# Kernel optimization log

Measured on AMD Instinct MI355X. Metric: run time of the kernel, lower is better.

Reference implementation:

```python
import jax, jax.numpy as jnp
import numpy as np

GROUPS = 32
EPS = 1e-6


def group_norm(x, gamma, beta):
    b, h, w, c = x.shape
    xg = x.reshape(b, h, w, GROUPS, c // GROUPS)
    mean = jnp.mean(xg, axis=(1, 2, 4), keepdims=True)
    var = jnp.var(xg, axis=(1, 2, 4), keepdims=True)
    xg = (xg - mean) * jax.lax.rsqrt(var + EPS)
    return xg.reshape(b, h, w, c) * gamma + beta


def setup_inputs() -> dict:
    key = jax.random.key(0)
    ks = jax.random.split(key, 6)
    B, H, W, C = 4, 64, 64, 512
    scale = 0.02
    return {
        "x": jax.random.normal(ks[0], (B, H, W, C), dtype=jnp.float32),
        "gamma": jnp.ones((C,), dtype=jnp.float32),
        "beta": jnp.zeros((C,), dtype=jnp.float32),
        "wq": jax.random.normal(ks[1], (C, C), dtype=jnp.float32) * scale,
        "bq": jnp.zeros((C,), dtype=jnp.float32),
        "wk": jax.random.normal(ks[2], (C, C), dtype=jnp.float32) * scale,
        "bk": jnp.zeros((C,), dtype=jnp.float32),
        "wv": jax.random.normal(ks[3], (C, C), dtype=jnp.float32) * scale,
        "bv": jnp.zeros((C,), dtype=jnp.float32),
        "wo": jax.random.normal(ks[4], (C, C), dtype=jnp.float32) * scale,
        "bo": jnp.zeros((C,), dtype=jnp.float32),
    }


def reference(x, gamma, beta, wq, bq, wk, bk, wv, bv, wo, bo):
    b, h, w, c = x.shape
    xn = group_norm(x, gamma, beta)
    # 1x1 convs == per-pixel linear layers
    q = (jnp.einsum('bhwc,cd->bhwd', xn, wq) + bq).reshape(b, h * w, c)
    k = (jnp.einsum('bhwc,cd->bhwd', xn, wk) + bk).reshape(b, h * w, c)
    v = (jnp.einsum('bhwc,cd->bhwd', xn, wv) + bv).reshape(b, h * w, c)
    # full (hw x hw) attention, single head
    scores = jnp.einsum('bic,bjc->bij', q, k) * (c ** -0.5)  # [b, hw, hw]
    attn = jax.nn.softmax(scores, axis=-1)
    out = jnp.einsum('bij,bjc->bic', attn, v).reshape(b, h, w, c)
    return jnp.einsum('bhwc,cd->bhwd', out, wo) + bo + x
```

## Files before the change

kernel.cpp:

```cpp
#include <hip/hip_runtime.h>
#include <stdint.h>


typedef __attribute__((ext_vector_type(8))) short bf16x8;
typedef __attribute__((ext_vector_type(8))) unsigned short u16x8;
typedef __attribute__((ext_vector_type(4))) float f32x4;

#define SOFTMAX_SCALE 0.044194173824159216f

__device__ __forceinline__ unsigned short f2bf(float f) {
  unsigned int x = __float_as_uint(f);
  x += 0x7fffu + ((x >> 16) & 1u);
  return (unsigned short)(x >> 16);
}
__device__ __forceinline__ float bf2f(unsigned short u) {
  return __uint_as_float((unsigned int)u << 16);
}

__device__ __forceinline__ void gl_lds16(const void* g, void* l) {
  __builtin_amdgcn_global_load_lds(
      (__attribute__((address_space(1))) unsigned char*)g,
      (__attribute__((address_space(3))) unsigned char*)l, 16, 0, 0);
}

__device__ __forceinline__ void gemm_tile(
    const unsigned short* __restrict__ A, long lda,
    const unsigned short* __restrict__ B, long ldb,
    int K, unsigned short* As, unsigned short* Bs, f32x4 acc[4][4]) {
  const int tid = threadIdx.x;
  const int wave = tid >> 6, lane = tid & 63;
  const int srow = lane >> 3;
  const int soff = ((lane & 7) ^ srow) * 16;
  const int wm = (wave >> 1) * 64, wn = (wave & 1) * 64;
  const int lrow = lane & 15;
  const int rsw = lrow & 7;
  const int kgb = lane >> 4;

  for (int k0 = 0; k0 < K; k0 += 64) {
    __syncthreads();
    for (int i = 0; i < 4; ++i) {
      int chunk = wave * 4 + i;
      int row = chunk * 8 + srow;
      gl_lds16((const char*)(A + (long)row * lda + k0) + soff, (char*)As + chunk * 1024);
      gl_lds16((const char*)(B + (long)row * ldb + k0) + soff, (char*)Bs + chunk * 1024);
    }
    __syncthreads();
#pragma unroll
    for (int ks = 0; ks < 2; ++ks) {
      bf16x8 af[4], bfr[4];
      const int off = ((ks * 4 + kgb) ^ rsw) * 8;
#pragma unroll
      for (int t = 0; t < 4; ++t) {
        af[t]  = *(const bf16x8*)&As[(wm + t * 16 + lrow) * 64 + off];
        bfr[t] = *(const bf16x8*)&Bs[(wn + t * 16 + lrow) * 64 + off];
      }
#pragma unroll
      for (int mt = 0; mt < 4; ++mt)
#pragma unroll
        for (int nt = 0; nt < 4; ++nt)
          acc[mt][nt] = __builtin_amdgcn_mfma_f32_16x16x32_bf16(af[mt], bfr[nt], acc[mt][nt], 0, 0, 0);
    }
  }
}

#define EPILOG_SETUP                                          \
  const int lane = threadIdx.x & 63, wave = threadIdx.x >> 6; \
  const int wm = (wave >> 1) * 64, wn = (wave & 1) * 64;      \
  const int lcol = lane & 15, lrb = (lane >> 4) * 4;

__global__ void prep_kernel(const float* __restrict__ wq, const float* __restrict__ wk,
                            const float* __restrict__ wv, const float* __restrict__ wo,
                            const float* __restrict__ bq, const float* __restrict__ bk,
                            const float* __restrict__ bv,
                            unsigned short* __restrict__ wqkvT,
                            unsigned short* __restrict__ woT,
                            float* __restrict__ bias, float* __restrict__ stats,
                            float* __restrict__ lsum) {
  long id = (long)blockIdx.x * 256 + threadIdx.x;
  if (id < 786432) {
    long n = id >> 9, k = id & 511;
    const float* w = (n < 512) ? wq : (n < 1024 ? wk : wv);
    wqkvT[id] = f2bf(w[k * 512 + (n & 511)]);
  } else if (id < 786432 + 262144) {
    long j = id - 786432, n = j >> 9, k = j & 511;
    woT[j] = f2bf(wo[k * 512 + n]);
  } else if (id < 786432 + 262144 + 1536) {
    long j = id - 786432 - 262144;
    bias[j] = (j < 512) ? bq[j] : (j < 1024 ? bk[j - 512] : bv[j - 1024]);
  } else if (id < 786432 + 262144 + 1536 + 256) {
    stats[id - 786432 - 262144 - 1536] = 0.f;
  } else if (id < 786432 + 262144 + 1536 + 256 + 16384) {
    lsum[id - 786432 - 262144 - 1536 - 256] = 0.f;
  }
}

__global__ __launch_bounds__(256) void gn_stats(const float* __restrict__ x,
                                                float* __restrict__ stats) {
  const int b = blockIdx.x >> 7, slab = blockIdx.x & 127;
  const float* xp = x + (long)b * 4096 * 512 + (long)slab * 32 * 512;
  const int tid = threadIdx.x;
  float s = 0.f, s2 = 0.f;
  for (int it = 0; it < 16; ++it) {
    int i = it * 256 + tid;
    float4 v = *(const float4*)(xp + (long)i * 4);
    s += v.x + v.y + v.z + v.w;
    s2 += v.x * v.x + v.y * v.y + v.z * v.z + v.w * v.w;
  }
  s += __shfl_xor(s, 1); s += __shfl_xor(s, 2);
  s2 += __shfl_xor(s2, 1); s2 += __shfl_xor(s2, 2);
  if ((tid & 3) == 0) {
    int g = (tid & 127) >> 2;
    atomicAdd(&stats[(b * 32 + g) * 2], s);
    atomicAdd(&stats[(b * 32 + g) * 2 + 1], s2);
  }
}

__global__ __launch_bounds__(256) void gn_apply(const float* __restrict__ x,
                                                const float* __restrict__ stats,
                                                const float* __restrict__ gamma,
                                                const float* __restrict__ beta,
                                                unsigned short* __restrict__ xn) {
  long id = (long)blockIdx.x * 256 + threadIdx.x;
  long a = id * 4;
  int b = (int)(id >> 19);
  int ch = (int)(a & 511);
  int g = ch >> 4;
  float s = stats[(b * 32 + g) * 2], s2 = stats[(b * 32 + g) * 2 + 1];
  float mean = s * (1.f / 65536.f);
  float rinv = rsqrtf(s2 * (1.f / 65536.f) - mean * mean + 1e-6f);
  float4 v = *(const float4*)(x + a);
  float4 gm = *(const float4*)(gamma + ch);
  float4 bt = *(const float4*)(beta + ch);
  ushort4 o;
  o.x = f2bf((v.x - mean) * rinv * gm.x + bt.x);
  o.y = f2bf((v.y - mean) * rinv * gm.y + bt.y);
  o.z = f2bf((v.z - mean) * rinv * gm.z + bt.z);
  o.w = f2bf((v.w - mean) * rinv * gm.w + bt.w);
  *(ushort4*)(xn + a) = o;
}

__global__ __launch_bounds__(256) void qkv_kernel(
    const unsigned short* __restrict__ xn, const unsigned short* __restrict__ wqkvT,
    const float* __restrict__ bias, unsigned short* __restrict__ q,
    unsigned short* __restrict__ kk, unsigned short* __restrict__ vv) {
  __shared__ unsigned short As[128 * 64], Bs[128 * 64];
  f32x4 acc[4][4] = {};
  const long tm = (long)blockIdx.x * 128, tn = (long)blockIdx.y * 128;
  gemm_tile(xn + tm * 512, 512, wqkvT + tn * 512, 512, 512, As, Bs, acc);
  EPILOG_SETUP
#pragma unroll
  for (int mt = 0; mt < 4; ++mt)
#pragma unroll
    for (int nt = 0; nt < 4; ++nt)
#pragma unroll
      for (int r = 0; r < 4; ++r) {
        long m = tm + wm + mt * 16 + lrb + r;
        long n = tn + wn + nt * 16 + lcol;
        float v = acc[mt][nt][r] + bias[n];
        if (n < 512)       q[m * 512 + n] = f2bf(v * SOFTMAX_SCALE);
        else if (n < 1024) kk[m * 512 + (n - 512)] = f2bf(v);
        else               vv[m * 512 + (n - 1024)] = f2bf(v);
      }
}

__global__ __launch_bounds__(256) void transpose_v(const unsigned short* __restrict__ v,
                                                   unsigned short* __restrict__ vT) {
  const int b = blockIdx.z;
  const long j0 = (long)blockIdx.x * 64, c0 = (long)blockIdx.y * 64;
  __shared__ unsigned short t[64][72];
  const int tc = (threadIdx.x & 15) * 4, tr = threadIdx.x >> 4;
  for (int rr = 0; rr < 64; rr += 16) {
    ushort4 u = *(const ushort4*)&v[((long)b * 4096 + j0 + tr + rr) * 512 + c0 + tc];
    t[tr + rr][tc] = u.x; t[tr + rr][tc + 1] = u.y;
    t[tr + rr][tc + 2] = u.z; t[tr + rr][tc + 3] = u.w;
  }
  __syncthreads();
  for (int rr = 0; rr < 64; rr += 16) {
    int c = tr + rr;
    ushort4 o;
    o.x = t[tc + 0][c]; o.y = t[tc + 1][c]; o.z = t[tc + 2][c]; o.w = t[tc + 3][c];
    *(ushort4*)&vT[((long)b * 512 + c0 + c) * 4096 + j0 + tc] = o;
  }
}

__global__ __launch_bounds__(256) void qkt_kernel(
    const unsigned short* __restrict__ q, const unsigned short* __restrict__ kk,
    unsigned short* __restrict__ probs, float* __restrict__ lsum, int b0) {
  __shared__ unsigned short As[128 * 64], Bs[128 * 64];
  f32x4 acc[4][4] = {};
  const int z = blockIdx.z;
  const long bb = (long)(b0 + z) * 4096 * 512;
  const long tm = (long)blockIdx.x * 128, tn = (long)blockIdx.y * 128;
  gemm_tile(q + bb + tm * 512, 512, kk + bb + tn * 512, 512, 512, As, Bs, acc);
  EPILOG_SETUP
  unsigned short* out = probs + (long)z * 4096 * 4096;
  float* ls = lsum + (long)(b0 + z) * 4096;
#pragma unroll
  for (int mt = 0; mt < 4; ++mt) {
    float rsum[4] = {0.f, 0.f, 0.f, 0.f};
#pragma unroll
    for (int nt = 0; nt < 4; ++nt)
#pragma unroll
      for (int r = 0; r < 4; ++r) {
        long m = tm + wm + mt * 16 + lrb + r;
        long n = tn + wn + nt * 16 + lcol;
        float e = __expf(acc[mt][nt][r]);
        unsigned short h = f2bf(e);
        out[m * 4096 + n] = h;
        rsum[r] += bf2f(h);
      }
#pragma unroll
    for (int r = 0; r < 4; ++r) {
      float s = rsum[r];
      s += __shfl_xor(s, 1); s += __shfl_xor(s, 2);
      s += __shfl_xor(s, 4); s += __shfl_xor(s, 8);
      if (lcol == 0) atomicAdd(&ls[tm + wm + mt * 16 + lrb + r], s);
    }
  }
}

__global__ __launch_bounds__(256) void pv_kernel(
    const unsigned short* __restrict__ probs, const unsigned short* __restrict__ vT,
    unsigned short* __restrict__ part, int b0) {
  __shared__ unsigned short As[128 * 64], Bs[128 * 64];
  f32x4 acc[4][4] = {};
  const int zb = blockIdx.z >> 2, s = blockIdx.z & 3;
  const long tm = (long)blockIdx.x * 128, tn = (long)blockIdx.y * 128;
  gemm_tile(probs + (long)zb * 4096 * 4096 + tm * 4096 + s * 1024, 4096,
            vT + (long)(b0 + zb) * 512 * 4096 + tn * 4096 + s * 1024, 4096,
            1024, As, Bs, acc);
  EPILOG_SETUP
  unsigned short* out = part + (long)blockIdx.z * 4096 * 512;
#pragma unroll
  for (int mt = 0; mt < 4; ++mt)
#pragma unroll
    for (int nt = 0; nt < 4; ++nt)
#pragma unroll
      for (int r = 0; r < 4; ++r) {
        long m = tm + wm + mt * 16 + lrb + r;
        long n = tn + wn + nt * 16 + lcol;
        out[m * 512 + n] = f2bf(acc[mt][nt][r]);
      }
}

__global__ __launch_bounds__(256) void reduce_kernel(const unsigned short* __restrict__ part,
                                                     const float* __restrict__ lsum,
                                                     unsigned short* __restrict__ attn,
                                                     int b0) {
  const long elems = 4096l * 512;
  const int zb = blockIdx.y;
  const unsigned short* pp = part + (long)zb * 4 * elems;
  long id = (long)blockIdx.x * 256 + threadIdx.x;
  long a = id * 8;
  int m = (int)(a >> 9);
  float inv = 1.f / lsum[(long)(b0 + zb) * 4096 + m];
  u16x8 p0 = *(const u16x8*)(pp + a);
  u16x8 p1 = *(const u16x8*)(pp + elems + a);
  u16x8 p2 = *(const u16x8*)(pp + 2 * elems + a);
  u16x8 p3 = *(const u16x8*)(pp + 3 * elems + a);
  u16x8 o;
#pragma unroll
  for (int j = 0; j < 8; ++j)
    o[j] = f2bf((bf2f(p0[j]) + bf2f(p1[j]) + bf2f(p2[j]) + bf2f(p3[j])) * inv);
  *(u16x8*)(attn + (long)(b0 + zb) * elems + a) = o;
}

__global__ __launch_bounds__(256) void proj_kernel(
    const unsigned short* __restrict__ attn, const unsigned short* __restrict__ woT,
    const float* __restrict__ bo, const float* __restrict__ x,
    float* __restrict__ out) {
  __shared__ unsigned short As[128 * 64], Bs[128 * 64];
  f32x4 acc[4][4] = {};
  const long tm = (long)blockIdx.x * 128, tn = (long)blockIdx.y * 128;
  gemm_tile(attn + tm * 512, 512, woT + tn * 512, 512, 512, As, Bs, acc);
  EPILOG_SETUP
#pragma unroll
  for (int mt = 0; mt < 4; ++mt)
#pragma unroll
    for (int nt = 0; nt < 4; ++nt)
#pragma unroll
      for (int r = 0; r < 4; ++r) {
        long m = tm + wm + mt * 16 + lrb + r;
        long n = tn + wn + nt * 16 + lcol;
        out[m * 512 + n] = acc[mt][nt][r] + bo[n] + x[m * 512 + n];
      }
}

extern "C" void kernel_launch(void* const* d_in, const int* in_sizes, int n_in,
                              void* d_out, int out_size, void* d_ws, size_t ws_size,
                              hipStream_t stream) {
  const float* x     = (const float*)d_in[0];
  const float* gamma = (const float*)d_in[1];
  const float* beta  = (const float*)d_in[2];
  const float* wq    = (const float*)d_in[3];
  const float* bq    = (const float*)d_in[4];
  const float* wk    = (const float*)d_in[5];
  const float* bk    = (const float*)d_in[6];
  const float* wv    = (const float*)d_in[7];
  const float* bv    = (const float*)d_in[8];
  const float* wo    = (const float*)d_in[9];
  const float* bo    = (const float*)d_in[10];

  char* p = (char*)d_ws;
  auto take = [&](size_t bytes) { char* r = p; p += (bytes + 255) & ~(size_t)255; return r; };
  const long NTOK = 16384, C = 512, HW = 4096;
  unsigned short* xn    = (unsigned short*)take(NTOK * C * 2);
  unsigned short* q     = (unsigned short*)take(NTOK * C * 2);
  unsigned short* kbuf  = (unsigned short*)take(NTOK * C * 2);
  unsigned short* vT    = (unsigned short*)take(NTOK * C * 2);
  unsigned short* wqkvT = (unsigned short*)take(1536l * 512 * 2);
  unsigned short* woT   = (unsigned short*)take(512l * 512 * 2);
  float* bias           = (float*)take(1536 * 4);
  float* stats          = (float*)take(256 * 4);
  float* lsum           = (float*)take(16384 * 4);

  size_t fixed = (size_t)(p - (char*)d_ws);
  size_t per_nb = (size_t)HW * HW * 2 + 4ul * HW * C * 2 + 512;
  int NB = (ws_size >= fixed + 4 * per_nb) ? 4
         : (ws_size >= fixed + 2 * per_nb) ? 2 : 1;
  unsigned short* probs = (unsigned short*)take((size_t)NB * HW * HW * 2);
  unsigned short* part  = (unsigned short*)take((size_t)NB * 4 * HW * C * 2);
  unsigned short* attn  = xn;
  unsigned short* vbuf  = part;

  prep_kernel<<<4168, 256, 0, stream>>>(wq, wk, wv, wo, bq, bk, bv, wqkvT, woT,
                                        bias, stats, lsum);
  gn_stats<<<512, 256, 0, stream>>>(x, stats);
  gn_apply<<<8192, 256, 0, stream>>>(x, stats, gamma, beta, xn);

  qkv_kernel<<<dim3(128, 12), 256, 0, stream>>>(xn, wqkvT, bias, q, kbuf, vbuf);
  transpose_v<<<dim3(64, 8, 4), 256, 0, stream>>>(vbuf, vT);

  for (int b0 = 0; b0 < 4; b0 += NB) {
    qkt_kernel<<<dim3(32, 32, NB), 256, 0, stream>>>(q, kbuf, probs, lsum, b0);
    pv_kernel<<<dim3(32, 4, 4 * NB), 256, 0, stream>>>(probs, vT, part, b0);
    reduce_kernel<<<dim3(1024, NB), 256, 0, stream>>>(part, lsum, attn, b0);
  }

  proj_kernel<<<dim3(128, 4), 256, 0, stream>>>(attn, woT, bo, x, (float*)d_out);
}
```

Before: 415.2 us.

## Fuse GN stats into prep kernel, use register-direct GEMM, exp2 softmax

Merges the weight-prep and group-norm statistics kernels into one launch and zeroes stats/lsum with a memset instead of kernel threads. The QK^T and output-projection GEMMs now load bf16 fragments straight from global memory into registers, skipping the LDS staging. The log2(e) factor is folded into the Q scale so the softmax can use exp2f. Dropping LDS removes barriers and shared-memory traffic but depends on L1/L2 caching for operand reuse across waves, which may cost more global traffic.

```diff
diff --git a/kernel.cpp b/kernel.cpp
--- a/kernel.cpp
+++ b/kernel.cpp
@@ -6,7 +6,7 @@
 typedef __attribute__((ext_vector_type(8))) unsigned short u16x8;
 typedef __attribute__((ext_vector_type(4))) float f32x4;
 
-#define SOFTMAX_SCALE 0.044194173824159216f
+#define QSCALE_LOG2E 0.06376435229f
 
 __device__ __forceinline__ unsigned short f2bf(float f) {
   unsigned int x = __float_as_uint(f);
@@ -63,20 +63,65 @@
   }
 }
 
+template <int K>
+__device__ __forceinline__ void gemm_reg(
+    const unsigned short* __restrict__ A, long lda,
+    const unsigned short* __restrict__ B, long ldb, f32x4 acc[4][4]) {
+  const int lane = threadIdx.x & 63, wave = threadIdx.x >> 6;
+  const int wm = (wave >> 1) * 64, wn = (wave & 1) * 64;
+  const int lr = lane & 15, kg = (lane >> 4) * 8;
+  const unsigned short* a0 = A + (long)(wm + lr) * lda + kg;
+  const unsigned short* b0 = B + (long)(wn + lr) * ldb + kg;
+#pragma unroll
+  for (int ks = 0; ks < K; ks += 32) {
+    bf16x8 af[4], bfr[4];
+#pragma unroll
+    for (int t = 0; t < 4; ++t) {
+      af[t]  = *(const bf16x8*)(a0 + (long)t * 16 * lda + ks);
+      bfr[t] = *(const bf16x8*)(b0 + (long)t * 16 * ldb + ks);
+    }
+#pragma unroll
+    for (int mt = 0; mt < 4; ++mt)
+#pragma unroll
+      for (int nt = 0; nt < 4; ++nt)
+        acc[mt][nt] = __builtin_amdgcn_mfma_f32_16x16x32_bf16(af[mt], bfr[nt], acc[mt][nt], 0, 0, 0);
+  }
+}
+
 #define EPILOG_SETUP                                          \
   const int lane = threadIdx.x & 63, wave = threadIdx.x >> 6; \
   const int wm = (wave >> 1) * 64, wn = (wave & 1) * 64;      \
   const int lcol = lane & 15, lrb = (lane >> 4) * 4;
 
-__global__ void prep_kernel(const float* __restrict__ wq, const float* __restrict__ wk,
-                            const float* __restrict__ wv, const float* __restrict__ wo,
-                            const float* __restrict__ bq, const float* __restrict__ bk,
-                            const float* __restrict__ bv,
-                            unsigned short* __restrict__ wqkvT,
-                            unsigned short* __restrict__ woT,
-                            float* __restrict__ bias, float* __restrict__ stats,
-                            float* __restrict__ lsum) {
-  long id = (long)blockIdx.x * 256 + threadIdx.x;
+__global__ __launch_bounds__(256) void prep_gn_kernel(
+    const float* __restrict__ x, float* __restrict__ stats,
+    const float* __restrict__ wq, const float* __restrict__ wk,
+    const float* __restrict__ wv, const float* __restrict__ wo,
+    const float* __restrict__ bq, const float* __restrict__ bk,
+    const float* __restrict__ bv,
+    unsigned short* __restrict__ wqkvT, unsigned short* __restrict__ woT,
+    float* __restrict__ bias) {
+  const int tid = threadIdx.x;
+  if (blockIdx.x < 512) {
+    const int b = blockIdx.x >> 7, slab = blockIdx.x & 127;
+    const float* xp = x + (long)b * 4096 * 512 + (long)slab * 32 * 512;
+    float s = 0.f, s2 = 0.f;
+    for (int it = 0; it < 16; ++it) {
+      int i = it * 256 + tid;
+      float4 v = *(const float4*)(xp + (long)i * 4);
+      s += v.x + v.y + v.z + v.w;
+      s2 += v.x * v.x + v.y * v.y + v.z * v.z + v.w * v.w;
+    }
+    s += __shfl_xor(s, 1); s += __shfl_xor(s, 2);
+    s2 += __shfl_xor(s2, 1); s2 += __shfl_xor(s2, 2);
+    if ((tid & 3) == 0) {
+      int g = (tid & 127) >> 2;
+      atomicAdd(&stats[(b * 32 + g) * 2], s);
+      atomicAdd(&stats[(b * 32 + g) * 2 + 1], s2);
+    }
+    return;
+  }
+  long id = (long)(blockIdx.x - 512) * 256 + tid;
   if (id < 786432) {
     long n = id >> 9, k = id & 511;
     const float* w = (n < 512) ? wq : (n < 1024 ? wk : wv);
@@ -87,31 +132,6 @@
   } else if (id < 786432 + 262144 + 1536) {
     long j = id - 786432 - 262144;
     bias[j] = (j < 512) ? bq[j] : (j < 1024 ? bk[j - 512] : bv[j - 1024]);
-  } else if (id < 786432 + 262144 + 1536 + 256) {
-    stats[id - 786432 - 262144 - 1536] = 0.f;
-  } else if (id < 786432 + 262144 + 1536 + 256 + 16384) {
-    lsum[id - 786432 - 262144 - 1536 - 256] = 0.f;
-  }
-}
-
-__global__ __launch_bounds__(256) void gn_stats(const float* __restrict__ x,
-                                                float* __restrict__ stats) {
-  const int b = blockIdx.x >> 7, slab = blockIdx.x & 127;
-  const float* xp = x + (long)b * 4096 * 512 + (long)slab * 32 * 512;
-  const int tid = threadIdx.x;
-  float s = 0.f, s2 = 0.f;
-  for (int it = 0; it < 16; ++it) {
-    int i = it * 256 + tid;
-    float4 v = *(const float4*)(xp + (long)i * 4);
-    s += v.x + v.y + v.z + v.w;
-    s2 += v.x * v.x + v.y * v.y + v.z * v.z + v.w * v.w;
-  }
-  s += __shfl_xor(s, 1); s += __shfl_xor(s, 2);
-  s2 += __shfl_xor(s2, 1); s2 += __shfl_xor(s2, 2);
-  if ((tid & 3) == 0) {
-    int g = (tid & 127) >> 2;
-    atomicAdd(&stats[(b * 32 + g) * 2], s);
-    atomicAdd(&stats[(b * 32 + g) * 2 + 1], s2);
   }
 }
 
@@ -157,7 +177,7 @@
         long m = tm + wm + mt * 16 + lrb + r;
         long n = tn + wn + nt * 16 + lcol;
         float v = acc[mt][nt][r] + bias[n];
-        if (n < 512)       q[m * 512 + n] = f2bf(v * SOFTMAX_SCALE);
+        if (n < 512)       q[m * 512 + n] = f2bf(v * QSCALE_LOG2E);
         else if (n < 1024) kk[m * 512 + (n - 512)] = f2bf(v);
         else               vv[m * 512 + (n - 1024)] = f2bf(v);
       }
@@ -186,12 +206,11 @@
 __global__ __launch_bounds__(256) void qkt_kernel(
     const unsigned short* __restrict__ q, const unsigned short* __restrict__ kk,
     unsigned short* __restrict__ probs, float* __restrict__ lsum, int b0) {
-  __shared__ unsigned short As[128 * 64], Bs[128 * 64];
   f32x4 acc[4][4] = {};
   const int z = blockIdx.z;
   const long bb = (long)(b0 + z) * 4096 * 512;
   const long tm = (long)blockIdx.x * 128, tn = (long)blockIdx.y * 128;
-  gemm_tile(q + bb + tm * 512, 512, kk + bb + tn * 512, 512, 512, As, Bs, acc);
+  gemm_reg<512>(q + bb + tm * 512, 512, kk + bb + tn * 512, 512, acc);
   EPILOG_SETUP
   unsigned short* out = probs + (long)z * 4096 * 4096;
   float* ls = lsum + (long)(b0 + z) * 4096;
@@ -204,7 +223,7 @@
       for (int r = 0; r < 4; ++r) {
         long m = tm + wm + mt * 16 + lrb + r;
         long n = tn + wn + nt * 16 + lcol;
-        float e = __expf(acc[mt][nt][r]);
+        float e = exp2f(acc[mt][nt][r]);
         unsigned short h = f2bf(e);
         out[m * 4096 + n] = h;
         rsum[r] += bf2f(h);
@@ -269,10 +288,9 @@
     const unsigned short* __restrict__ attn, const unsigned short* __restrict__ woT,
     const float* __restrict__ bo, const float* __restrict__ x,
     float* __restrict__ out) {
-  __shared__ unsigned short As[128 * 64], Bs[128 * 64];
   f32x4 acc[4][4] = {};
   const long tm = (long)blockIdx.x * 128, tn = (long)blockIdx.y * 128;
-  gemm_tile(attn + tm * 512, 512, woT + tn * 512, 512, 512, As, Bs, acc);
+  gemm_reg<512>(attn + tm * 512, 512, woT + tn * 512, 512, acc);
   EPILOG_SETUP
 #pragma unroll
   for (int mt = 0; mt < 4; ++mt)
@@ -323,9 +341,9 @@
   unsigned short* attn  = xn;
   unsigned short* vbuf  = part;
 
-  prep_kernel<<<4168, 256, 0, stream>>>(wq, wk, wv, wo, bq, bk, bv, wqkvT, woT,
-                                        bias, stats, lsum);
-  gn_stats<<<512, 256, 0, stream>>>(x, stats);
+  hipMemsetAsync(stats, 0, (size_t)((char*)(lsum + 16384) - (char*)stats), stream);
+  prep_gn_kernel<<<512 + 4103, 256, 0, stream>>>(x, stats, wq, wk, wv, wo,
+                                                 bq, bk, bv, wqkvT, woT, bias);
   gn_apply<<<8192, 256, 0, stream>>>(x, stats, gamma, beta, xn);
 
   qkv_kernel<<<dim3(128, 12), 256, 0, stream>>>(xn, wqkvT, bias, q, kbuf, vbuf);
```

Result: slower. 583.8 us (+40.6%).
